# Performance work log

Hardware: AMD Instinct MI355X
Metric: run time of the kernel (lower is better)

The kernel has to match this reference:

```python
import jax, jax.numpy as jnp
import numpy as np

N, NFEAT, NFEAT_EXT, NHID, NCLASS, NHEADS = 8192, 512, 128, 256, 10, 8


def setup_inputs() -> dict:
    key = jax.random.key(0)
    ks = jax.random.split(key, 12)
    s = lambda fan_in: 1.0 / np.sqrt(fan_in)
    return {
        "x": jax.random.normal(ks[0], (N, NFEAT), jnp.float32),
        "adj": jax.random.uniform(ks[1], (N, N), jnp.float32) / N,  # row-stochastic-ish normalized adjacency
        "sub_fea": jax.random.normal(ks[2], (1, NFEAT_EXT), jnp.float32),
        # GraphConvolution 1: nfeat -> nhid
        "gc1_W": jax.random.normal(ks[3], (NFEAT, NHID), jnp.float32) * s(NFEAT),
        "gc1_b": jnp.zeros((NHID,), jnp.float32),
        # GraphConvolution 2: nhid -> 2*nhid
        "gc2_W": jax.random.normal(ks[4], (NHID, 2 * NHID), jnp.float32) * s(NHID),
        "gc2_b": jnp.zeros((2 * NHID,), jnp.float32),
        # fc1: nfeat_ext -> nhid
        "fc1_W": jax.random.normal(ks[5], (NFEAT_EXT, NHID), jnp.float32) * s(NFEAT_EXT),
        "fc1_b": jnp.zeros((NHID,), jnp.float32),
        # AttentionLayer(3*nhid, nclass, nheads): per-head projection + softmax head gating
        "att_W": jax.random.normal(ks[6], (NHEADS, 3 * NHID, NCLASS), jnp.float32) * s(3 * NHID),
        "att_a": jax.random.normal(ks[7], (NHEADS, 3 * NHID), jnp.float32) * s(3 * NHID),
        "att_b": jnp.zeros((NCLASS,), jnp.float32),
    }


def reference(x, adj, sub_fea, gc1_W, gc1_b, gc2_W, gc2_b, fc1_W, fc1_b, att_W, att_a, att_b):
    # GCN layer 1: adj @ (x @ W) + b, then ReLU
    h = jax.nn.relu(adj @ (x @ gc1_W) + gc1_b)            # [N, nhid]
    # GCN layer 2
    h = jax.nn.relu(adj @ (h @ gc2_W) + gc2_b)            # [N, 2*nhid]
    # global_mean_pool(batch=None): mean over all nodes -> single graph vector
    g = jax.nn.selu(jnp.mean(h, axis=0, keepdims=True))    # [1, 2*nhid]
    # dropout is identity in eval mode
    x_ext = sub_fea @ fc1_W + fc1_b                        # [1, nhid]
    z = jnp.concatenate([g, x_ext], axis=1)                # [1, 3*nhid]
    # multi-head attention fusion: softmax over head scores gating per-head projections
    scores = jnp.einsum("bi,hi->bh", z, att_a)            # [1, nheads]
    alpha = jax.nn.softmax(scores, axis=1)
    head_out = jnp.einsum("bi,hio->bho", z, att_W)        # [1, nheads, nclass]
    out = jnp.einsum("bh,bho->bo", alpha, head_out) + att_b  # [1, nclass]
    return jax.nn.log_softmax(out, axis=1)
```

## Files before the change

kernel.cpp:

```cpp
#include <hip/hip_runtime.h>

typedef __attribute__((ext_vector_type(8))) short short8;
typedef __attribute__((ext_vector_type(4))) float floatx4;
typedef unsigned short ushort_t;

__device__ __forceinline__ ushort_t f2bf(float x) {
  union { float f; unsigned int u; } v; v.f = x;
  unsigned int u = v.u;
  return (ushort_t)((u + 0x7FFFu + ((u >> 16) & 1u)) >> 16);
}
__device__ __forceinline__ unsigned int pk2(float a, float b) {
  return (unsigned int)f2bf(a) | ((unsigned int)f2bf(b) << 16);
}

__global__ void prep_kernel(const float* __restrict__ W1, const float* __restrict__ W2,
                            ushort_t* __restrict__ W1T, ushort_t* __restrict__ W2T) {
  int idx = blockIdx.x * 256 + threadIdx.x;
  if (idx < 256 * 512) {
    int n = idx >> 9, k = idx & 511;
    W1T[idx] = f2bf(W1[k * 256 + n]);
    int n2 = idx >> 8, k2 = idx & 255;
    W2T[idx] = f2bf(W2[k2 * 512 + n2]);
  }
}

template<bool ABF, bool BBF, int EPI>
__global__ __launch_bounds__(256, 2)
void gemm128(const void* __restrict__ Ap, const void* __restrict__ Bp,
             const float* __restrict__ bias, void* __restrict__ Cv,
             float* __restrict__ gacc, const int K, const int N) {
  __shared__ ushort_t Als[4096];
  __shared__ ushort_t Bls[4096];

  const int t = threadIdx.x;
  const int lane = t & 63;
  const int w = t >> 6;
  const int wm = w >> 1, wn = w & 1;
  const int ml = lane & 15, quad = lane >> 4;
  const int m0 = blockIdx.y * 128, n0 = blockIdx.x * 128;
  const int sr = t >> 1, sh = t & 1;

  const int Kper = K / gridDim.z;
  const int kbeg = blockIdx.z * Kper;

  long aoff = (long)(m0 + sr) * K + kbeg + sh * 16;
  long boff = (long)(n0 + sr) * K + kbeg + sh * 16;

  const float*    Af = (const float*)Ap;
  const ushort_t* Ab = (const ushort_t*)Ap;
  const float*    Bf = (const float*)Bp;
  const ushort_t* Bb = (const ushort_t*)Bp;

  floatx4 acc[4][4] = {};

  const int lw0 = ((2 * sh) * 128 + sr) * 8;
  const int lw1 = ((2 * sh + 1) * 128 + sr) * 8;

  uint4 aU0, aU1, bU0, bU1;
  float4 aF0, aF1, aF2, aF3, bF0, bF1, bF2, bF3;

  auto loadA = [&]() {
    if constexpr (ABF) {
      aU0 = *(const uint4*)(Ab + aoff);
      aU1 = *(const uint4*)(Ab + aoff + 8);
    } else {
      aF0 = *(const float4*)(Af + aoff);
      aF1 = *(const float4*)(Af + aoff + 4);
      aF2 = *(const float4*)(Af + aoff + 8);
      aF3 = *(const float4*)(Af + aoff + 12);
    }
    aoff += 32;
  };
  auto loadB = [&]() {
    if constexpr (BBF) {
      bU0 = *(const uint4*)(Bb + boff);
      bU1 = *(const uint4*)(Bb + boff + 8);
    } else {
      bF0 = *(const float4*)(Bf + boff);
      bF1 = *(const float4*)(Bf + boff + 4);
      bF2 = *(const float4*)(Bf + boff + 8);
      bF3 = *(const float4*)(Bf + boff + 12);
    }
    boff += 32;
  };

  loadA();
  loadB();

  for (int kk = 0; kk < Kper; kk += 32) {
    uint4 a0, a1, b0, b1;
    if constexpr (ABF) { a0 = aU0; a1 = aU1; }
    else {
      a0 = make_uint4(pk2(aF0.x,aF0.y), pk2(aF0.z,aF0.w), pk2(aF1.x,aF1.y), pk2(aF1.z,aF1.w));
      a1 = make_uint4(pk2(aF2.x,aF2.y), pk2(aF2.z,aF2.w), pk2(aF3.x,aF3.y), pk2(aF3.z,aF3.w));
    }
    if constexpr (BBF) { b0 = bU0; b1 = bU1; }
    else {
      b0 = make_uint4(pk2(bF0.x,bF0.y), pk2(bF0.z,bF0.w), pk2(bF1.x,bF1.y), pk2(bF1.z,bF1.w));
      b1 = make_uint4(pk2(bF2.x,bF2.y), pk2(bF2.z,bF2.w), pk2(bF3.x,bF3.y), pk2(bF3.z,bF3.w));
    }
    __syncthreads();
    *(uint4*)(Als + lw0) = a0;
    *(uint4*)(Als + lw1) = a1;
    *(uint4*)(Bls + lw0) = b0;
    *(uint4*)(Bls + lw1) = b1;
    if (kk + 32 < Kper) {
      loadA();
      loadB();
    }
    __syncthreads();

    short8 av[4], bv[4];
#pragma unroll
    for (int f = 0; f < 4; ++f) {
      av[f] = *(const short8*)(Als + (quad * 128 + wm * 64 + f * 16 + ml) * 8);
      bv[f] = *(const short8*)(Bls + (quad * 128 + wn * 64 + f * 16 + ml) * 8);
    }
#pragma unroll
    for (int fm = 0; fm < 4; ++fm)
#pragma unroll
      for (int fn = 0; fn < 4; ++fn)
        acc[fm][fn] = __builtin_amdgcn_mfma_f32_16x16x32_bf16(av[fm], bv[fn], acc[fm][fn], 0, 0, 0);
  }

  if constexpr (EPI == 2) {
#pragma unroll
    for (int fm = 0; fm < 4; ++fm) {
      int rowb = m0 + wm * 64 + fm * 16 + quad * 4;
#pragma unroll
      for (int r = 0; r < 4; ++r) {
        float bb = bias[rowb + r];
        float s = 0.f;
#pragma unroll
        for (int fn = 0; fn < 4; ++fn)
          s += fmaxf(acc[fm][fn][r] + bb, 0.f);
        s += __shfl_xor(s, 1);
        s += __shfl_xor(s, 2);
        s += __shfl_xor(s, 4);
        s += __shfl_xor(s, 8);
        if (ml == 0) atomicAdd(gacc + rowb + r, s);
      }
    }
  } else if constexpr (EPI == 3) {
    float* Cf = (float*)Cv;
    const long zoff = (long)blockIdx.z * ((long)gridDim.y * 128) * N;
#pragma unroll
    for (int fm = 0; fm < 4; ++fm)
#pragma unroll
      for (int fn = 0; fn < 4; ++fn) {
        int gm = m0 + wm * 64 + fm * 16 + quad * 4;
        int gn = n0 + wn * 64 + fn * 16 + ml;
#pragma unroll
        for (int r = 0; r < 4; ++r)
          Cf[zoff + (long)(gm + r) * N + gn] = acc[fm][fn][r];
      }
  } else {
    ushort_t* C = (ushort_t*)Cv;
#pragma unroll
    for (int fm = 0; fm < 4; ++fm)
#pragma unroll
      for (int fn = 0; fn < 4; ++fn) {
        int gm = m0 + wm * 64 + fm * 16 + quad * 4;
        int gn = n0 + wn * 64 + fn * 16 + ml;
#pragma unroll
        for (int r = 0; r < 4; ++r) {
          float v = acc[fm][fn][r];
          if constexpr (EPI == 1) v = fmaxf(v + bias[gm + r], 0.f);
          C[(long)(gm + r) * N + gn] = f2bf(v);
        }
      }
  }
}

template<bool RELU_BIAS>
__global__ void reduceZ_kernel(const float* __restrict__ p, ushort_t* __restrict__ out,
                               const float* __restrict__ bias, const int rowShift,
                               const long total4, const long zstride, const int Z) {
  long i = (long)blockIdx.x * blockDim.x + threadIdx.x;
  if (i >= total4) return;
  long e = i * 4;
  float4 s = *(const float4*)(p + e);
  for (int z = 1; z < Z; ++z) {
    float4 b = *(const float4*)(p + (long)z * zstride + e);
    s.x += b.x; s.y += b.y; s.z += b.z; s.w += b.w;
  }
  if constexpr (RELU_BIAS) {
    float bb = bias[e >> rowShift];
    s.x = fmaxf(s.x + bb, 0.f); s.y = fmaxf(s.y + bb, 0.f);
    s.z = fmaxf(s.z + bb, 0.f); s.w = fmaxf(s.w + bb, 0.f);
  }
  uint2 o;
  o.x = pk2(s.x, s.y);
  o.y = pk2(s.z, s.w);
  *(uint2*)(out + e) = o;
}

__global__ void tail_kernel(const float* __restrict__ gacc, const float* __restrict__ sub_fea,
                            const float* __restrict__ fc1_W, const float* __restrict__ fc1_b,
                            const float* __restrict__ att_W, const float* __restrict__ att_a,
                            const float* __restrict__ att_b, float* __restrict__ out) {
  __shared__ float z[768];
  __shared__ float sc[8];
  __shared__ float alpha[8];
  __shared__ float outsh[10];
  const int t = threadIdx.x;

  for (int j = t; j < 512; j += 256) {
    float x = gacc[j] * (1.0f / 8192.0f);
    const float scale = 1.0507009873554805f, al = 1.6732632423543772f;
    z[j] = x > 0.f ? scale * x : scale * al * (expf(x) - 1.0f);
  }
  {
    float a = fc1_b[t];
    for (int i = 0; i < 128; ++i) a += sub_fea[i] * fc1_W[i * 256 + t];
    z[512 + t] = a;
  }
  if (t < 10) outsh[t] = 0.f;
  __syncthreads();

  {
    int h = t >> 5, ln = t & 31;
    float p = 0.f;
    for (int i = ln; i < 768; i += 32) p += z[i] * att_a[h * 768 + i];
    for (int m = 16; m; m >>= 1) p += __shfl_down(p, m, 32);
    if (ln == 0) sc[h] = p;
  }
  __syncthreads();
  if (t == 0) {
    float mx = sc[0];
    for (int h = 1; h < 8; ++h) mx = fmaxf(mx, sc[h]);
    float s = 0.f, e[8];
    for (int h = 0; h < 8; ++h) { e[h] = expf(sc[h] - mx); s += e[h]; }
    for (int h = 0; h < 8; ++h) alpha[h] = e[h] / s;
  }
  __syncthreads();

  float p[10];
#pragma unroll
  for (int o = 0; o < 10; ++o) p[o] = 0.f;
  for (int i = t; i < 768; i += 256) {
    float zi = z[i];
    for (int h = 0; h < 8; ++h) {
      float za = zi * alpha[h];
      const float* wp = att_W + (h * 768 + i) * 10;
#pragma unroll
      for (int o = 0; o < 10; ++o) p[o] += za * wp[o];
    }
  }
#pragma unroll
  for (int o = 0; o < 10; ++o) atomicAdd(&outsh[o], p[o]);
  __syncthreads();
  if (t == 0) {
    float v[10], mx = -1e30f;
    for (int o = 0; o < 10; ++o) { v[o] = outsh[o] + att_b[o]; mx = fmaxf(mx, v[o]); }
    float s = 0.f;
    for (int o = 0; o < 10; ++o) s += expf(v[o] - mx);
    float lse = logf(s) + mx;
    for (int o = 0; o < 10; ++o) out[o] = v[o] - lse;
  }
}

extern "C" void kernel_launch(void* const* d_in, const int* in_sizes, int n_in,
                              void* d_out, int out_size, void* d_ws, size_t ws_size,
                              hipStream_t stream) {
  const float* x       = (const float*)d_in[0];
  const float* adj     = (const float*)d_in[1];
  const float* sub_fea = (const float*)d_in[2];
  const float* gc1_W   = (const float*)d_in[3];
  const float* gc1_b   = (const float*)d_in[4];
  const float* gc2_W   = (const float*)d_in[5];
  const float* gc2_b   = (const float*)d_in[6];
  const float* fc1_W   = (const float*)d_in[7];
  const float* fc1_b   = (const float*)d_in[8];
  const float* att_W   = (const float*)d_in[9];
  const float* att_a   = (const float*)d_in[10];
  const float* att_b   = (const float*)d_in[11];
  float* out = (float*)d_out;

  const int zbig = (ws_size >= (size_t)(90u << 20)) ? 8 : 2;

  char* ws = (char*)d_ws;
  const size_t MB = 1u << 20;
  ushort_t* t1T  = (ushort_t*)(ws);
  ushort_t* h1T  = (ushort_t*)(ws + 4 * MB);
  ushort_t* P    = (ushort_t*)(ws + 8 * MB);
  float*    part = (float*)   (ws + 12 * MB);
  size_t    partBytes = (size_t)zbig * 2097152 * 4;
  ushort_t* W1T  = (ushort_t*)(ws + 12 * MB + partBytes);
  ushort_t* W2T  = (ushort_t*)(ws + 12 * MB + partBytes + 262144);
  float*    gacc = (float*)   (ws + 12 * MB + partBytes + 524288);

  hipMemsetAsync(gacc, 0, 512 * sizeof(float), stream);
  prep_kernel<<<512, 256, 0, stream>>>(gc1_W, gc2_W, W1T, W2T);

  gemm128<true, false, 3><<<dim3(64, 2, 2), 256, 0, stream>>>(W1T, x, nullptr, part, nullptr, 512, 8192);
  reduceZ_kernel<false><<<2048, 256, 0, stream>>>(part, t1T, nullptr, 0, 524288L, 2097152L, 2);

  gemm128<true, false, 3><<<dim3(64, 2, zbig), 256, 0, stream>>>(t1T, adj, nullptr, part, nullptr, 8192, 8192);
  reduceZ_kernel<true><<<2048, 256, 0, stream>>>(part, h1T, gc1_b, 13, 524288L, 2097152L, zbig);

  gemm128<false, true, 3><<<dim3(2, 64, zbig), 256, 0, stream>>>(adj, h1T, nullptr, part, nullptr, 8192, 256);
  reduceZ_kernel<false><<<2048, 256, 0, stream>>>(part, P, nullptr, 0, 524288L, 2097152L, zbig);

  gemm128<true, true, 2><<<dim3(64, 4, 1), 256, 0, stream>>>(W2T, P, gc2_b, nullptr, gacc, 256, 8192);

  tail_kernel<<<1, 256, 0, stream>>>(gacc, sub_fea, fc1_W, fc1_b, att_W, att_a, att_b, out);
}
```

Baseline: 688.1 us.

## Pre-convert adj and x to bf16 and use 256-wide tiles for adj GEMMs

Adds a conversion kernel that writes adj and x to bf16 once when the workspace is large enough, so the two adjacency GEMMs read half the bytes and skip per-tile fp32 packing. The GEMM kernel is templated on tile shape, and the adj GEMMs now use 256x128 or 128x256 tiles covering all output columns, so adj is streamed once per GEMM instead of twice. Split-K is fixed at 8. The cost is an extra full pass over adj to convert it, a larger workspace requirement, and more registers per thread for the bigger tiles.

```diff
diff --git a/kernel.cpp b/kernel.cpp
--- a/kernel.cpp
+++ b/kernel.cpp
@@ -24,115 +24,150 @@
   }
 }
 
-template<bool ABF, bool BBF, int EPI>
+__global__ void cvt2_kernel(const float* __restrict__ s1, ushort_t* __restrict__ d1, long n1_8,
+                            const float* __restrict__ s2, ushort_t* __restrict__ d2, long n2_8) {
+  long i = (long)blockIdx.x * 256 + threadIdx.x;
+  const float* s; ushort_t* d; long e;
+  if (i < n1_8) { s = s1; d = d1; e = i * 8; }
+  else { i -= n1_8; if (i >= n2_8) return; s = s2; d = d2; e = i * 8; }
+  float4 a = *(const float4*)(s + e);
+  float4 b = *(const float4*)(s + e + 4);
+  uint4 o = make_uint4(pk2(a.x, a.y), pk2(a.z, a.w), pk2(b.x, b.y), pk2(b.z, b.w));
+  *(uint4*)(d + e) = o;
+}
+
+template<int MT, int NT, bool ABF, bool BBF, int EPI>
 __global__ __launch_bounds__(256, 2)
-void gemm128(const void* __restrict__ Ap, const void* __restrict__ Bp,
+void gemm_bf(const void* __restrict__ Ap, const void* __restrict__ Bp,
              const float* __restrict__ bias, void* __restrict__ Cv,
              float* __restrict__ gacc, const int K, const int N) {
-  __shared__ ushort_t Als[4096];
-  __shared__ ushort_t Bls[4096];
+  static_assert(MT == 128 || MT == 256, "");
+  static_assert(NT == 128 || NT == 256, "");
+  static_assert(MT * NT <= 128 * 256, "");
+  static_assert(ABF || MT == 128, "");
+  static_assert(BBF || NT == 128, "");
+  constexpr int MF = MT / 32, NF = NT / 32;
+  constexpr int ACH = (MT == 256) ? 4 : 2;
+  constexpr int BCH = (NT == 256) ? 4 : 2;
+
+  __shared__ ushort_t Als[MT * 32];
+  __shared__ ushort_t Bls[NT * 32];
 
   const int t = threadIdx.x;
   const int lane = t & 63;
   const int w = t >> 6;
   const int wm = w >> 1, wn = w & 1;
   const int ml = lane & 15, quad = lane >> 4;
-  const int m0 = blockIdx.y * 128, n0 = blockIdx.x * 128;
-  const int sr = t >> 1, sh = t & 1;
-
+  const int m0 = blockIdx.y * MT, n0 = blockIdx.x * NT;
   const int Kper = K / gridDim.z;
   const int kbeg = blockIdx.z * Kper;
 
-  long aoff = (long)(m0 + sr) * K + kbeg + sh * 16;
-  long boff = (long)(n0 + sr) * K + kbeg + sh * 16;
-
-  const float*    Af = (const float*)Ap;
-  const ushort_t* Ab = (const ushort_t*)Ap;
-  const float*    Bf = (const float*)Bp;
-  const ushort_t* Bb = (const ushort_t*)Bp;
-
-  floatx4 acc[4][4] = {};
-
-  const int lw0 = ((2 * sh) * 128 + sr) * 8;
-  const int lw1 = ((2 * sh + 1) * 128 + sr) * 8;
-
-  uint4 aU0, aU1, bU0, bU1;
-  float4 aF0, aF1, aF2, aF3, bF0, bF1, bF2, bF3;
+  const ushort_t* Ab = (const ushort_t*)Ap; const float* Af = (const float*)Ap;
+  const ushort_t* Bb = (const ushort_t*)Bp; const float* Bf = (const float*)Bp;
+
+  long aoff = (MT == 256) ? ((long)(m0 + t) * K + kbeg)
+                          : ((long)(m0 + (t >> 1)) * K + kbeg + (t & 1) * 16);
+  long boff = (NT == 256) ? ((long)(n0 + t) * K + kbeg)
+                          : ((long)(n0 + (t >> 1)) * K + kbeg + (t & 1) * 16);
+
+  floatx4 acc[MF][NF] = {};
+
+  uint4 aS[ACH], bS[BCH];
+  float4 aF[4], bF[4];
 
   auto loadA = [&]() {
     if constexpr (ABF) {
-      aU0 = *(const uint4*)(Ab + aoff);
-      aU1 = *(const uint4*)(Ab + aoff + 8);
-    } else {
-      aF0 = *(const float4*)(Af + aoff);
-      aF1 = *(const float4*)(Af + aoff + 4);
-      aF2 = *(const float4*)(Af + aoff + 8);
-      aF3 = *(const float4*)(Af + aoff + 12);
+#pragma unroll
+      for (int c = 0; c < ACH; ++c) aS[c] = *(const uint4*)(Ab + aoff + 8 * c);
+    } else {
+#pragma unroll
+      for (int c = 0; c < 4; ++c) aF[c] = *(const float4*)(Af + aoff + 4 * c);
     }
     aoff += 32;
   };
   auto loadB = [&]() {
     if constexpr (BBF) {
-      bU0 = *(const uint4*)(Bb + boff);
-      bU1 = *(const uint4*)(Bb + boff + 8);
-    } else {
-      bF0 = *(const float4*)(Bf + boff);
-      bF1 = *(const float4*)(Bf + boff + 4);
-      bF2 = *(const float4*)(Bf + boff + 8);
-      bF3 = *(const float4*)(Bf + boff + 12);
+#pragma unroll
+      for (int c = 0; c < BCH; ++c) bS[c] = *(const uint4*)(Bb + boff + 8 * c);
+    } else {
+#pragma unroll
+      for (int c = 0; c < 4; ++c) bF[c] = *(const float4*)(Bf + boff + 4 * c);
     }
     boff += 32;
   };
-
-  loadA();
-  loadB();
-
-  for (int kk = 0; kk < Kper; kk += 32) {
-    uint4 a0, a1, b0, b1;
-    if constexpr (ABF) { a0 = aU0; a1 = aU1; }
-    else {
-      a0 = make_uint4(pk2(aF0.x,aF0.y), pk2(aF0.z,aF0.w), pk2(aF1.x,aF1.y), pk2(aF1.z,aF1.w));
-      a1 = make_uint4(pk2(aF2.x,aF2.y), pk2(aF2.z,aF2.w), pk2(aF3.x,aF3.y), pk2(aF3.z,aF3.w));
-    }
-    if constexpr (BBF) { b0 = bU0; b1 = bU1; }
-    else {
-      b0 = make_uint4(pk2(bF0.x,bF0.y), pk2(bF0.z,bF0.w), pk2(bF1.x,bF1.y), pk2(bF1.z,bF1.w));
-      b1 = make_uint4(pk2(bF2.x,bF2.y), pk2(bF2.z,bF2.w), pk2(bF3.x,bF3.y), pk2(bF3.z,bF3.w));
-    }
+  auto stageA = [&]() {
+    uint4 wv[ACH];
+    if constexpr (ABF) {
+#pragma unroll
+      for (int c = 0; c < ACH; ++c) wv[c] = aS[c];
+    } else {
+      wv[0] = make_uint4(pk2(aF[0].x, aF[0].y), pk2(aF[0].z, aF[0].w),
+                         pk2(aF[1].x, aF[1].y), pk2(aF[1].z, aF[1].w));
+      wv[1] = make_uint4(pk2(aF[2].x, aF[2].y), pk2(aF[2].z, aF[2].w),
+                         pk2(aF[3].x, aF[3].y), pk2(aF[3].z, aF[3].w));
+    }
+    if constexpr (MT == 256) {
+#pragma unroll
+      for (int c = 0; c < 4; ++c) *(uint4*)(Als + ((c * 256 + t) * 8)) = wv[c];
+    } else {
+      const int row = t >> 1, h = t & 1;
+      *(uint4*)(Als + (((2 * h) * 128 + row) * 8)) = wv[0];
+      *(uint4*)(Als + (((2 * h + 1) * 128 + row) * 8)) = wv[1];
+    }
+  };
+  auto stageB = [&]() {
+    uint4 wv[BCH];
+    if constexpr (BBF) {
+#pragma unroll
+      for (int c = 0; c < BCH; ++c) wv[c] = bS[c];
+    } else {
+      wv[0] = make_uint4(pk2(bF[0].x, bF[0].y), pk2(bF[0].z, bF[0].w),
+                         pk2(bF[1].x, bF[1].y), pk2(bF[1].z, bF[1].w));
+      wv[1] = make_uint4(pk2(bF[2].x, bF[2].y), pk2(bF[2].z, bF[2].w),
+                         pk2(bF[3].x, bF[3].y), pk2(bF[3].z, bF[3].w));
+    }
+    if constexpr (NT == 256) {
+#pragma unroll
+      for (int c = 0; c < 4; ++c) *(uint4*)(Bls + ((c * 256 + t) * 8)) = wv[c];
+    } else {
+      const int row = t >> 1, h = t & 1;
+      *(uint4*)(Bls + (((2 * h) * 128 + row) * 8)) = wv[0];
+      *(uint4*)(Bls + (((2 * h + 1) * 128 + row) * 8)) = wv[1];
+    }
+  };
+
+  loadA(); loadB();
+  const int iters = Kper >> 5;
+  for (int it = 0; it < iters; ++it) {
     __syncthreads();
-    *(uint4*)(Als + lw0) = a0;
-    *(uint4*)(Als + lw1) = a1;
-    *(uint4*)(Bls + lw0) = b0;
-    *(uint4*)(Bls + lw1) = b1;
-    if (kk + 32 < Kper) {
-      loadA();
-      loadB();
-    }
+    stageA(); stageB();
+    if (it + 1 < iters) { loadA(); loadB(); }
     __syncthreads();
 
-    short8 av[4], bv[4];
-#pragma unroll
-    for (int f = 0; f < 4; ++f) {
-      av[f] = *(const short8*)(Als + (quad * 128 + wm * 64 + f * 16 + ml) * 8);
-      bv[f] = *(const short8*)(Bls + (quad * 128 + wn * 64 + f * 16 + ml) * 8);
-    }
-#pragma unroll
-    for (int fm = 0; fm < 4; ++fm)
-#pragma unroll
-      for (int fn = 0; fn < 4; ++fn)
+    short8 av[MF], bv[NF];
+#pragma unroll
+    for (int f = 0; f < MF; ++f)
+      av[f] = *(const short8*)(Als + (quad * MT + wm * (MT / 2) + f * 16 + ml) * 8);
+#pragma unroll
+    for (int f = 0; f < NF; ++f)
+      bv[f] = *(const short8*)(Bls + (quad * NT + wn * (NT / 2) + f * 16 + ml) * 8);
+#pragma unroll
+    for (int fm = 0; fm < MF; ++fm)
+#pragma unroll
+      for (int fn = 0; fn < NF; ++fn)
         acc[fm][fn] = __builtin_amdgcn_mfma_f32_16x16x32_bf16(av[fm], bv[fn], acc[fm][fn], 0, 0, 0);
   }
 
   if constexpr (EPI == 2) {
 #pragma unroll
-    for (int fm = 0; fm < 4; ++fm) {
-      int rowb = m0 + wm * 64 + fm * 16 + quad * 4;
+    for (int fm = 0; fm < MF; ++fm) {
+      int rowb = m0 + wm * (MT / 2) + fm * 16 + quad * 4;
 #pragma unroll
       for (int r = 0; r < 4; ++r) {
         float bb = bias[rowb + r];
         float s = 0.f;
 #pragma unroll
-        for (int fn = 0; fn < 4; ++fn)
+        for (int fn = 0; fn < NF; ++fn)
           s += fmaxf(acc[fm][fn][r] + bb, 0.f);
         s += __shfl_xor(s, 1);
         s += __shfl_xor(s, 2);
@@ -143,13 +178,13 @@
     }
   } else if constexpr (EPI == 3) {
     float* Cf = (float*)Cv;
-    const long zoff = (long)blockIdx.z * ((long)gridDim.y * 128) * N;
-#pragma unroll
-    for (int fm = 0; fm < 4; ++fm)
-#pragma unroll
-      for (int fn = 0; fn < 4; ++fn) {
-        int gm = m0 + wm * 64 + fm * 16 + quad * 4;
-        int gn = n0 + wn * 64 + fn * 16 + ml;
+    const long zoff = (long)blockIdx.z * (long)(gridDim.y * MT) * N;
+#pragma unroll
+    for (int fm = 0; fm < MF; ++fm)
+#pragma unroll
+      for (int fn = 0; fn < NF; ++fn) {
+        int gm = m0 + wm * (MT / 2) + fm * 16 + quad * 4;
+        int gn = n0 + wn * (NT / 2) + fn * 16 + ml;
 #pragma unroll
         for (int r = 0; r < 4; ++r)
           Cf[zoff + (long)(gm + r) * N + gn] = acc[fm][fn][r];
@@ -157,17 +192,14 @@
   } else {
     ushort_t* C = (ushort_t*)Cv;
 #pragma unroll
-    for (int fm = 0; fm < 4; ++fm)
-#pragma unroll
-      for (int fn = 0; fn < 4; ++fn) {
-        int gm = m0 + wm * 64 + fm * 16 + quad * 4;
-        int gn = n0 + wn * 64 + fn * 16 + ml;
-#pragma unroll
-        for (int r = 0; r < 4; ++r) {
-          float v = acc[fm][fn][r];
-          if constexpr (EPI == 1) v = fmaxf(v + bias[gm + r], 0.f);
-          C[(long)(gm + r) * N + gn] = f2bf(v);
-        }
+    for (int fm = 0; fm < MF; ++fm)
+#pragma unroll
+      for (int fn = 0; fn < NF; ++fn) {
+        int gm = m0 + wm * (MT / 2) + fm * 16 + quad * 4;
+        int gn = n0 + wn * (NT / 2) + fn * 16 + ml;
+#pragma unroll
+        for (int r = 0; r < 4; ++r)
+          C[(long)(gm + r) * N + gn] = f2bf(acc[fm][fn][r]);
       }
   }
 }
@@ -277,32 +309,52 @@
   const float* att_b   = (const float*)d_in[11];
   float* out = (float*)d_out;
 
-  const int zbig = (ws_size >= (size_t)(90u << 20)) ? 8 : 2;
+  const size_t MB = 1u << 20;
+  const bool big = ws_size >= 224 * MB;
 
   char* ws = (char*)d_ws;
-  const size_t MB = 1u << 20;
-  ushort_t* t1T  = (ushort_t*)(ws);
-  ushort_t* h1T  = (ushort_t*)(ws + 4 * MB);
-  ushort_t* P    = (ushort_t*)(ws + 8 * MB);
-  float*    part = (float*)   (ws + 12 * MB);
-  size_t    partBytes = (size_t)zbig * 2097152 * 4;
-  ushort_t* W1T  = (ushort_t*)(ws + 12 * MB + partBytes);
-  ushort_t* W2T  = (ushort_t*)(ws + 12 * MB + partBytes + 262144);
-  float*    gacc = (float*)   (ws + 12 * MB + partBytes + 524288);
+  size_t off = 0;
+  ushort_t* adjbf = (ushort_t*)(ws); if (big) off += 128 * MB;
+  ushort_t* xbf   = (ushort_t*)(ws + off); off += 8 * MB;
+  ushort_t* t1T   = (ushort_t*)(ws + off); off += 4 * MB;
+  ushort_t* h1T   = (ushort_t*)(ws + off); off += 4 * MB;
+  ushort_t* P     = (ushort_t*)(ws + off); off += 4 * MB;
+  float*    part  = (float*)   (ws + off); off += 64 * MB;
+  ushort_t* W1T   = (ushort_t*)(ws + off); off += 262144;
+  ushort_t* W2T   = (ushort_t*)(ws + off); off += 262144;
+  float*    gacc  = (float*)   (ws + off);
 
   hipMemsetAsync(gacc, 0, 512 * sizeof(float), stream);
   prep_kernel<<<512, 256, 0, stream>>>(gc1_W, gc2_W, W1T, W2T);
 
-  gemm128<true, false, 3><<<dim3(64, 2, 2), 256, 0, stream>>>(W1T, x, nullptr, part, nullptr, 512, 8192);
+  if (big) {
+    cvt2_kernel<<<32768 + 2048, 256, 0, stream>>>(adj, adjbf, 8388608L, x, xbf, 524288L);
+  } else {
+    cvt2_kernel<<<2048, 256, 0, stream>>>(x, xbf, 524288L, x, xbf, 0L);
+  }
+
+  gemm_bf<128, 128, true, true, 3><<<dim3(64, 2, 2), 256, 0, stream>>>(
+      W1T, xbf, nullptr, part, nullptr, 512, 8192);
   reduceZ_kernel<false><<<2048, 256, 0, stream>>>(part, t1T, nullptr, 0, 524288L, 2097152L, 2);
 
-  gemm128<true, false, 3><<<dim3(64, 2, zbig), 256, 0, stream>>>(t1T, adj, nullptr, part, nullptr, 8192, 8192);
-  reduceZ_kernel<true><<<2048, 256, 0, stream>>>(part, h1T, gc1_b, 13, 524288L, 2097152L, zbig);
-
-  gemm128<false, true, 3><<<dim3(2, 64, zbig), 256, 0, stream>>>(adj, h1T, nullptr, part, nullptr, 8192, 256);
-  reduceZ_kernel<false><<<2048, 256, 0, stream>>>(part, P, nullptr, 0, 524288L, 2097152L, zbig);
-
-  gemm128<true, true, 2><<<dim3(64, 4, 1), 256, 0, stream>>>(W2T, P, gc2_b, nullptr, gacc, 256, 8192);
+  if (big)
+    gemm_bf<256, 128, true, true, 3><<<dim3(64, 1, 8), 256, 0, stream>>>(
+        t1T, adjbf, nullptr, part, nullptr, 8192, 8192);
+  else
+    gemm_bf<256, 128, true, false, 3><<<dim3(64, 1, 8), 256, 0, stream>>>(
+        t1T, adj, nullptr, part, nullptr, 8192, 8192);
+  reduceZ_kernel<true><<<2048, 256, 0, stream>>>(part, h1T, gc1_b, 13, 524288L, 2097152L, 8);
+
+  if (big)
+    gemm_bf<128, 256, true, true, 3><<<dim3(1, 64, 8), 256, 0, stream>>>(
+        adjbf, h1T, nullptr, part, nullptr, 8192, 256);
+  else
+    gemm_bf<128, 256, false, true, 3><<<dim3(1, 64, 8), 256, 0, stream>>>(
+        adj, h1T, nullptr, part, nullptr, 8192, 256);
+  reduceZ_kernel<false><<<2048, 256, 0, stream>>>(part, P, nullptr, 0, 524288L, 2097152L, 8);
+
+  gemm_bf<128, 128, true, true, 2><<<dim3(64, 4, 1), 256, 0, stream>>>(
+      W2T, P, gc2_b, nullptr, gacc, 256, 8192);
 
   tail_kernel<<<1, 256, 0, stream>>>(gacc, sub_fea, fc1_W, fc1_b, att_W, att_a, att_b, out);
 }
```

Result: slower. 875.3 us (+27.2%).
